# Kernel optimization log

Hardware: AMD Instinct MI355X
Metric: run time of the kernel (lower is better)

Reference implementation:

```python
import jax, jax.numpy as jnp
import numpy as np

HIDDEN = 1024
NUM_HEADS = 16
HEAD_DIM = HIDDEN // NUM_HEADS


def rotary_cos_sin(seq_len, head_dim, dtype=jnp.float32):
    inv_freq = 1.0 / (10000.0 ** (jnp.arange(0, head_dim, 2, dtype=dtype) / head_dim))
    t = jnp.arange(seq_len, dtype=dtype)
    freqs = jnp.einsum('i,j->ij', t, inv_freq)          # [S, hd/2]
    emb = jnp.concatenate([freqs, freqs], axis=-1)      # [S, hd]
    return jnp.cos(emb), jnp.sin(emb)


def apply_rotary(x, cos, sin):
    # x: [B, H, S, hd]; cos/sin: [S, hd]
    x1, x2 = jnp.split(x, 2, axis=-1)
    x_rot = jnp.concatenate([-x2, x1], axis=-1)
    return x * cos + x_rot * sin


def setup_inputs() -> dict:
    key = jax.random.key(0)
    ks = jax.random.split(key, 5)
    S, B = 2048, 2
    x = jax.random.normal(ks[0], (S, B, HIDDEN), dtype=jnp.float32)
    s = 1.0 / np.sqrt(HIDDEN)
    W_qkv = jax.random.uniform(ks[1], (HIDDEN, 3 * HIDDEN), jnp.float32, -s, s)
    b_qkv = jax.random.uniform(ks[2], (3 * HIDDEN,), jnp.float32, -s, s)
    W_out = jax.random.uniform(ks[3], (HIDDEN, HIDDEN), jnp.float32, -s, s)
    b_out = jax.random.uniform(ks[4], (HIDDEN,), jnp.float32, -s, s)
    return {"x": x, "W_qkv": W_qkv, "b_qkv": b_qkv, "W_out": W_out, "b_out": b_out}


def reference(x, W_qkv, b_qkv, W_out, b_out):
    S, B, D = x.shape
    scale = HEAD_DIM ** -0.5
    qkv = x @ W_qkv + b_qkv                               # [S, B, 3D]
    qkv = qkv.reshape(S, B, NUM_HEADS, 3 * HEAD_DIM)
    q, k, v = jnp.split(qkv, 3, axis=-1)                  # each [S, B, H, hd]
    q = q.transpose(1, 2, 0, 3)                           # [B, H, S, hd]
    k = k.transpose(1, 2, 0, 3)
    v = v.transpose(1, 2, 0, 3)
    cos, sin = rotary_cos_sin(S, HEAD_DIM, x.dtype)
    q = apply_rotary(q, cos, sin)
    k = apply_rotary(k, cos, sin)
    scores = jnp.einsum('bhqd,bhkd->bhqk', q, k) * scale  # [B, H, S, S]
    weights = jax.nn.softmax(scores, axis=-1)
    attn = jnp.einsum('bhqk,bhkd->bhqd', weights, v)      # [B, H, S, hd]
    attn = attn.transpose(2, 0, 1, 3).reshape(S, B, D)    # [S, B, D]
    return attn @ W_out + b_out
```

## Files before the change

kernel.cpp:

```cpp
#include <hip/hip_runtime.h>

typedef unsigned short u16;
typedef __attribute__((ext_vector_type(8))) short bf16x8;
typedef __attribute__((ext_vector_type(4))) float f32x4;
typedef __attribute__((ext_vector_type(16))) float f32x16;

#define S_LEN 2048
#define BATCH 2
#define HID 1024
#define NH 16
#define HD 64
#define MROWS 4096
#define QKV_N 3072
#define QSCALE 0.18033688011112042f

__device__ __forceinline__ u16 f2bf(float f) {
  unsigned u = __float_as_uint(f);
  u += 0x7fffu + ((u >> 16) & 1u);
  return (u16)(u >> 16);
}

__device__ __forceinline__ float bf2f(u16 u) {
  return __uint_as_float((unsigned)u << 16);
}

__device__ __forceinline__ float fexp2(float x) {
  float r; asm("v_exp_f32 %0, %1" : "=v"(r) : "v"(x)); return r;
}

__device__ __forceinline__ unsigned cvtpk(float lo, float hi) {
  unsigned r; asm("v_cvt_pk_bf16_f32 %0, %1, %2" : "=v"(r) : "v"(lo), "v"(hi)); return r;
}

__device__ __forceinline__ void gl2lds16(const u16* src, u16* lds) {
  __builtin_amdgcn_global_load_lds((__attribute__((address_space(1))) void*)(void*)src,
                                   (__attribute__((address_space(3))) void*)(void*)lds,
                                   16, 0, 0);
}

__device__ __forceinline__ void castT_body(const float* __restrict__ W, u16* __restrict__ Wt,
                                           int Ncols, int Krows, int bx, int by,
                                           float (*tile)[33]) {
  int c0 = bx * 32, r0 = by * 32;
  int tx = threadIdx.x & 31, ty = threadIdx.x >> 5;
  #pragma unroll
  for (int i = 0; i < 4; ++i)
    tile[ty + i * 8][tx] = W[(size_t)(r0 + ty + i * 8) * Ncols + c0 + tx];
  __syncthreads();
  #pragma unroll
  for (int i = 0; i < 4; ++i) {
    int a = ty + i * 8;
    Wt[(size_t)(c0 + a) * Krows + r0 + tx] = f2bf(tile[tx][a]);
  }
}

__global__ __launch_bounds__(256) void prep(
    const float* __restrict__ x, const float* __restrict__ W_qkv,
    const float* __restrict__ W_out, u16* __restrict__ xb,
    u16* __restrict__ Wqt, u16* __restrict__ Wot, float2* __restrict__ rope) {
  __shared__ float tile[32][33];
  const int bid = blockIdx.x;
  if (bid < 2048) {
    int i = bid * 256 + threadIdx.x;
    const float4* p = (const float4*)x;
    float4 a = p[2 * i], b = p[2 * i + 1];
    union { u16 us[8]; uint4 v; } o;
    o.us[0] = f2bf(a.x); o.us[1] = f2bf(a.y); o.us[2] = f2bf(a.z); o.us[3] = f2bf(a.w);
    o.us[4] = f2bf(b.x); o.us[5] = f2bf(b.y); o.us[6] = f2bf(b.z); o.us[7] = f2bf(b.w);
    *(uint4*)&xb[8 * i] = o.v;
  } else if (bid < 2048 + 3072) {
    int r = bid - 2048;
    castT_body(W_qkv, Wqt, QKV_N, HID, r % 96, r / 96, tile);
  } else if (bid < 2048 + 3072 + 1024) {
    int r = bid - (2048 + 3072);
    castT_body(W_out, Wot, HID, HID, r % 32, r / 32, tile);
  } else {
    int i = (bid - 6144) * 256 + threadIdx.x;
    int s = i >> 5, j = i & 31;
    float invf = fexp2(-(float)(2 * j) * (13.287712379549449f / 64.0f));
    float ang = (float)s * invf;
    rope[i] = make_float2(cosf(ang), sinf(ang));
  }
}

__global__ __launch_bounds__(256, 2) void gemm_qkv(
    const u16* __restrict__ A, const u16* __restrict__ Bt,
    const float* __restrict__ bias, const float2* __restrict__ rope,
    u16* __restrict__ Qb, u16* __restrict__ Kb, u16* __restrict__ VtOut) {
  __shared__ u16 As[128 * 32];
  __shared__ u16 Bs[128 * 32];
  __shared__ u16 vt[2][64][64];
  const int tid = threadIdx.x;
  const int lane = tid & 63, wid = tid >> 6;
  const int g = lane >> 4, l15 = lane & 15;
  const int bm0 = blockIdx.x * 128, bn0 = blockIdx.y * 128;
  const int wm = wid >> 1, wn = wid & 1;

  f32x4 acc[4][4] = {};
  for (int kt = 0; kt < 32; ++kt) {
    const int k0 = kt * 32;
    __syncthreads();
    #pragma unroll
    for (int it = 0; it < 2; ++it) {
      int s = it * 256 + tid;
      gl2lds16(A  + (size_t)(bm0 + (s >> 2)) * 1024 + k0 + (s & 3) * 8, &As[s * 8]);
      gl2lds16(Bt + (size_t)(bn0 + (s >> 2)) * 1024 + k0 + (s & 3) * 8, &Bs[s * 8]);
    }
    __syncthreads();
    bf16x8 af[4], bfr[4];
    #pragma unroll
    for (int m = 0; m < 4; ++m) af[m]  = *(const bf16x8*)&As[(wm * 64 + m * 16 + l15) * 32 + g * 8];
    #pragma unroll
    for (int n = 0; n < 4; ++n) bfr[n] = *(const bf16x8*)&Bs[(wn * 64 + n * 16 + l15) * 32 + g * 8];
    #pragma unroll
    for (int m = 0; m < 4; ++m)
      #pragma unroll
      for (int n = 0; n < 4; ++n)
        acc[m][n] = __builtin_amdgcn_mfma_f32_16x16x32_bf16(af[m], bfr[n], acc[m][n], 0, 0, 0);
  }

  const int cw0 = bn0 + wn * 64;
  const int gi = cw0 >> 6;
  const int h = gi / 3, tt = gi % 3;
  float bs[4];
  #pragma unroll
  for (int n = 0; n < 4; ++n) bs[n] = bias[cw0 + n * 16 + l15];
  const size_t hb = (size_t)h * (S_LEN * HD);

  if (tt == 2) {
    #pragma unroll
    for (int m = 0; m < 4; ++m)
      #pragma unroll
      for (int reg = 0; reg < 4; ++reg) {
        int rl = wm * 64 + m * 16 + g * 4 + reg;
        int srow = rl >> 1, b = reg & 1;
        #pragma unroll
        for (int n = 0; n < 4; ++n) {
          int d = n * 16 + l15;
          vt[b][d][srow ^ ((d & 7) << 3)] = f2bf(acc[m][n][reg] + bs[n]);
        }
      }
  } else {
    u16* dst = (tt == 0) ? Qb : Kb;
    const float scl = (tt == 0) ? QSCALE : 1.0f;
    #pragma unroll
    for (int m = 0; m < 4; ++m)
      #pragma unroll
      for (int reg = 0; reg < 4; ++reg) {
        int r = bm0 + wm * 64 + m * 16 + g * 4 + reg;
        int srow = r >> 1, b = r & 1;
        size_t o = (size_t)(b * NH) * (S_LEN * HD) + hb + (size_t)srow * HD;
        #pragma unroll
        for (int n = 0; n < 2; ++n) {
          int dlo = n * 16 + l15;
          float2 cs = rope[srow * 32 + dlo];
          float v1 = acc[m][n][reg] + bs[n];
          float v2 = acc[m][n + 2][reg] + bs[n + 2];
          dst[o + dlo]      = f2bf((v1 * cs.x - v2 * cs.y) * scl);
          dst[o + dlo + 32] = f2bf((v2 * cs.x + v1 * cs.y) * scl);
        }
      }
  }
  __syncthreads();
  if (tt == 2) {
    const int vtid = wm * 64 + lane;
    const int s0g = bm0 >> 1;
    #pragma unroll
    for (int it = 0; it < 8; ++it) {
      int task = vtid + it * 128;
      int b = task >> 9, d = (task >> 3) & 63, ch = task & 7;
      uint4 v = *(const uint4*)&vt[b][d][(ch ^ (d & 7)) * 8];
      *(uint4*)&VtOut[((size_t)(b * NH + h) * HD + d) * S_LEN + s0g + ch * 8] = v;
    }
  }
}

__global__ __launch_bounds__(512, 4) void attn_fwd(
    const u16* __restrict__ Qb, const u16* __restrict__ Kb,
    const u16* __restrict__ Vt, u16* __restrict__ part0,
    u16* __restrict__ part1, float2* __restrict__ stats) {
  __shared__ u16 Ks[2][64 * 64];
  __shared__ u16 Vs[2][64 * 64];
  const int tid = threadIdx.x;
  const int lane = tid & 63, wid = tid >> 6;
  const int l31 = lane & 31, h = lane >> 5;
  const int pp = blockIdx.x & 63;
  const int bh = pp >> 1, split = pp & 1;
  const int kt0 = split * 16;
  const int qw0 = (blockIdx.x >> 6) * 256 + wid * 32;
  const u16* Qp = Qb + ((size_t)bh * S_LEN + qw0) * HD;
  const u16* Kp = Kb + (size_t)bh * S_LEN * HD;
  const u16* Vp = Vt + (size_t)bh * HD * S_LEN;

  const int sr = tid >> 3, tc = tid & 7;
  const int ssw = tc ^ (sr & 7);
  const int act = ((sr >> 4) & 1) * 16 + ((sr >> 2) & 1) * 8
                + ((sr & 3) | (((sr >> 3) & 1) << 2)) + (sr >> 5) * 32;
  const u16* kg = Kp + (size_t)act * HD + ssw * 8;
  const u16* vg = Vp + (size_t)sr * S_LEN + ssw * 8;

  bf16x8 qf0 = *(const bf16x8*)&Qp[(size_t)l31 * HD +  0 + h * 8];
  bf16x8 qf1 = *(const bf16x8*)&Qp[(size_t)l31 * HD + 16 + h * 8];
  bf16x8 qf2 = *(const bf16x8*)&Qp[(size_t)l31 * HD + 32 + h * 8];
  bf16x8 qf3 = *(const bf16x8*)&Qp[(size_t)l31 * HD + 48 + h * 8];

  f32x16 po0 = {}, po1 = {};
  float mrun = -INFINITY, lrun = 0.f;

  gl2lds16(kg + (size_t)kt0 * 64 * HD, &Ks[0][tid * 8]);
  gl2lds16(vg + kt0 * 64, &Vs[0][tid * 8]);
  __syncthreads();

  for (int i = 0; i < 16; ++i) {
    const int bb = i & 1;
    if (i + 1 < 16) {
      gl2lds16(kg + (size_t)(kt0 + i + 1) * 64 * HD, &Ks[bb ^ 1][tid * 8]);
      gl2lds16(vg + (kt0 + i + 1) * 64, &Vs[bb ^ 1][tid * 8]);
    }
    const u16* KsB = Ks[bb];
    const u16* VsB = Vs[bb];

    f32x16 s0 = {}, s1 = {};
    __builtin_amdgcn_s_setprio(1);
    #pragma unroll
    for (int s = 0; s < 4; ++s) {
      const bf16x8 qf = (s == 0) ? qf0 : (s == 1) ? qf1 : (s == 2) ? qf2 : qf3;
      const int csw = ((2 * s + h) ^ (l31 & 7)) * 8;
      bf16x8 kf0 = *(const bf16x8*)&KsB[l31 * 64 + csw];
      s0 = __builtin_amdgcn_mfma_f32_32x32x16_bf16(kf0, qf, s0, 0, 0, 0);
      bf16x8 kf1 = *(const bf16x8*)&KsB[(32 + l31) * 64 + csw];
      s1 = __builtin_amdgcn_mfma_f32_32x32x16_bf16(kf1, qf, s1, 0, 0, 0);
    }
    __builtin_amdgcn_s_setprio(0);

    float tm = -INFINITY;
    #pragma unroll
    for (int r = 0; r < 16; ++r) tm = fmaxf(tm, fmaxf(s0[r], s1[r]));
    tm = fmaxf(tm, __shfl_xor(tm, 32));

    if (!__all(tm <= mrun + 8.f)) {
      float mnew = fmaxf(mrun, tm);
      float alpha = fexp2(mrun - mnew);
      mrun = mnew;
      lrun *= alpha;
      #pragma unroll
      for (int r = 0; r < 16; ++r) {
        float ar = __shfl(alpha, (r & 3) + 8 * (r >> 2) + 4 * h);
        po0[r] *= ar;
        po1[r] *= ar;
      }
    }

    float rs = 0.f;
    unsigned pwa[8], pwb[8];
    #pragma unroll
    for (int w = 0; w < 8; ++w) {
      float a = fexp2(s0[2 * w] - mrun), bq = fexp2(s0[2 * w + 1] - mrun);
      rs += a + bq;
      pwa[w] = cvtpk(a, bq);
    }
    #pragma unroll
    for (int w = 0; w < 8; ++w) {
      float a = fexp2(s1[2 * w] - mrun), bq = fexp2(s1[2 * w + 1] - mrun);
      rs += a + bq;
      pwb[w] = cvtpk(a, bq);
    }
    rs += __shfl_xor(rs, 32);
    lrun += rs;

    __builtin_amdgcn_s_setprio(1);
    #pragma unroll
    for (int s = 0; s < 4; ++s) {
      union { unsigned w[4]; bf16x8 v; } pf;
      if (s == 0)      { pf.w[0] = pwa[0]; pf.w[1] = pwa[1]; pf.w[2] = pwa[2]; pf.w[3] = pwa[3]; }
      else if (s == 1) { pf.w[0] = pwa[4]; pf.w[1] = pwa[5]; pf.w[2] = pwa[6]; pf.w[3] = pwa[7]; }
      else if (s == 2) { pf.w[0] = pwb[0]; pf.w[1] = pwb[1]; pf.w[2] = pwb[2]; pf.w[3] = pwb[3]; }
      else             { pf.w[0] = pwb[4]; pf.w[1] = pwb[5]; pf.w[2] = pwb[6]; pf.w[3] = pwb[7]; }
      const int csw = ((2 * s + h) ^ (l31 & 7)) * 8;
      bf16x8 vf0 = *(const bf16x8*)&VsB[l31 * 64 + csw];
      po0 = __builtin_amdgcn_mfma_f32_32x32x16_bf16(pf.v, vf0, po0, 0, 0, 0);
      bf16x8 vf1 = *(const bf16x8*)&VsB[(32 + l31) * 64 + csw];
      po1 = __builtin_amdgcn_mfma_f32_32x32x16_bf16(pf.v, vf1, po1, 0, 0, 0);
    }
    __builtin_amdgcn_s_setprio(0);
    __syncthreads();
  }

  u16* part = split ? part1 : part0;
  if (h == 0)
    stats[(size_t)split * (32 * 2048) + (size_t)bh * 2048 + qw0 + l31] =
        make_float2(mrun, lrun);
  #pragma unroll
  for (int r = 0; r < 16; ++r) {
    int q = qw0 + (r & 3) + 8 * (r >> 2) + 4 * h;
    size_t o = ((size_t)bh * 2048 + q) * 64 + l31;
    part[o]      = f2bf(po0[r]);
    part[o + 32] = f2bf(po1[r]);
  }
}

__global__ void attn_combine(const u16* __restrict__ part0, const u16* __restrict__ part1,
                             const float2* __restrict__ stats, u16* __restrict__ attn2d) {
  int t = blockIdx.x * 256 + threadIdx.x;
  int bh = t >> 14, r = t & 16383, q = r >> 3, dc = r & 7;
  int b = bh >> 4, h = bh & 15;
  float2 s0 = stats[bh * 2048 + q];
  float2 s1 = stats[32 * 2048 + bh * 2048 + q];
  float M = fmaxf(s0.x, s1.x);
  float w0 = fexp2(s0.x - M), w1 = fexp2(s1.x - M);
  float inv = 1.f / (w0 * s0.y + w1 * s1.y);
  w0 *= inv; w1 *= inv;
  size_t off = ((size_t)bh * 2048 + q) * 64 + dc * 8;
  union { uint4 v; u16 us[8]; } a, c, o;
  a.v = *(const uint4*)&part0[off];
  c.v = *(const uint4*)&part1[off];
  #pragma unroll
  for (int j = 0; j < 8; ++j)
    o.us[j] = f2bf(w0 * bf2f(a.us[j]) + w1 * bf2f(c.us[j]));
  *(uint4*)&attn2d[((size_t)q * BATCH + b) * HID + h * HD + dc * 8] = o.v;
}

__global__ __launch_bounds__(256, 4) void gemm_out(
    const u16* __restrict__ A, const u16* __restrict__ Bt,
    const float* __restrict__ bias, float* __restrict__ out) {
  __shared__ u16 As[64 * 32];
  __shared__ u16 Bs[64 * 32];
  const int tid = threadIdx.x;
  const int lane = tid & 63, wid = tid >> 6;
  const int g = lane >> 4, l15 = lane & 15;
  const int bm0 = blockIdx.x * 64, bn0 = blockIdx.y * 64;

  f32x4 acc[4] = {};
  for (int kt = 0; kt < 32; ++kt) {
    const int k0 = kt * 32;
    __syncthreads();
    gl2lds16(A  + (size_t)(bm0 + (tid >> 2)) * 1024 + k0 + (tid & 3) * 8, &As[tid * 8]);
    gl2lds16(Bt + (size_t)(bn0 + (tid >> 2)) * 1024 + k0 + (tid & 3) * 8, &Bs[tid * 8]);
    __syncthreads();
    bf16x8 af = *(const bf16x8*)&As[(wid * 16 + l15) * 32 + g * 8];
    bf16x8 bfr[4];
    #pragma unroll
    for (int n = 0; n < 4; ++n) bfr[n] = *(const bf16x8*)&Bs[(n * 16 + l15) * 32 + g * 8];
    #pragma unroll
    for (int n = 0; n < 4; ++n)
      acc[n] = __builtin_amdgcn_mfma_f32_16x16x32_bf16(af, bfr[n], acc[n], 0, 0, 0);
  }
  #pragma unroll
  for (int n = 0; n < 4; ++n) {
    int c = bn0 + n * 16 + l15;
    float bv = bias[c];
    #pragma unroll
    for (int reg = 0; reg < 4; ++reg) {
      int r = bm0 + wid * 16 + g * 4 + reg;
      out[(size_t)r * HID + c] = acc[n][reg] + bv;
    }
  }
}

extern "C" void kernel_launch(void* const* d_in, const int* in_sizes, int n_in,
                              void* d_out, int out_size, void* d_ws, size_t ws_size,
                              hipStream_t stream) {
  const float* x     = (const float*)d_in[0];
  const float* W_qkv = (const float*)d_in[1];
  const float* b_qkv = (const float*)d_in[2];
  const float* W_out = (const float*)d_in[3];
  const float* b_out = (const float*)d_in[4];
  float* out = (float*)d_out;

  char* ws = (char*)d_ws;
  size_t off = 0;
  auto carve = [&](size_t bytes) { void* p = ws + off; off += (bytes + 255) & ~(size_t)255; return p; };
  u16* xb      = (u16*)carve((size_t)MROWS * HID * 2);
  u16* Wqt     = (u16*)carve((size_t)QKV_N * HID * 2);
  u16* Wot     = (u16*)carve((size_t)HID * HID * 2);
  float2* rope = (float2*)carve((size_t)S_LEN * 32 * 8);
  u16* Qb      = (u16*)carve((size_t)BATCH * NH * S_LEN * HD * 2);
  u16* Kb      = (u16*)carve((size_t)BATCH * NH * S_LEN * HD * 2);
  u16* part1   = (u16*)carve((size_t)BATCH * NH * S_LEN * HD * 2);
  u16* Vt      = (u16*)carve((size_t)BATCH * NH * S_LEN * HD * 2);
  u16* attn2d  = (u16*)carve((size_t)MROWS * HID * 2);
  float2* stats= (float2*)carve((size_t)2 * 32 * 2048 * 8);

  prep<<<6400, 256, 0, stream>>>(x, W_qkv, W_out, xb, Wqt, Wot, rope);
  gemm_qkv<<<dim3(MROWS / 128, QKV_N / 128), 256, 0, stream>>>(xb, Wqt, b_qkv, rope, Qb, Kb, Vt);
  attn_fwd<<<512, 512, 0, stream>>>(Qb, Kb, Vt, xb, part1, stats);
  attn_combine<<<2048, 256, 0, stream>>>(xb, part1, stats, attn2d);
  gemm_out<<<dim3(MROWS / 64, HID / 64), 256, 0, stream>>>(attn2d, Wot, b_out, out);
}
```

Before: 120.7 us.

## Fuse split-KV combine into attention kernel via last-block atomic counter

Removes the separate attn_combine launch. Each attention block bumps an atomic counter per (query block, head), and whichever of the two split blocks finishes last merges both partial outputs and writes attn2d. Counters are zeroed in the prep kernel's rope blocks. This saves a kernel launch and its tail, but adds fences, an atomic, and a serialized combine tail on half of the blocks.

```diff
diff --git a/kernel.cpp b/kernel.cpp
--- a/kernel.cpp
+++ b/kernel.cpp
@@ -57,7 +57,8 @@
 __global__ __launch_bounds__(256) void prep(
     const float* __restrict__ x, const float* __restrict__ W_qkv,
     const float* __restrict__ W_out, u16* __restrict__ xb,
-    u16* __restrict__ Wqt, u16* __restrict__ Wot, float2* __restrict__ rope) {
+    u16* __restrict__ Wqt, u16* __restrict__ Wot, float2* __restrict__ rope,
+    int* __restrict__ flags) {
   __shared__ float tile[32][33];
   const int bid = blockIdx.x;
   if (bid < 2048) {
@@ -80,6 +81,7 @@
     float invf = fexp2(-(float)(2 * j) * (13.287712379549449f / 64.0f));
     float ang = (float)s * invf;
     rope[i] = make_float2(cosf(ang), sinf(ang));
+    if (threadIdx.x == 0) flags[bid - 6144] = 0;
   }
 }
 
@@ -178,16 +180,20 @@
 __global__ __launch_bounds__(512, 4) void attn_fwd(
     const u16* __restrict__ Qb, const u16* __restrict__ Kb,
     const u16* __restrict__ Vt, u16* __restrict__ part0,
-    u16* __restrict__ part1, float2* __restrict__ stats) {
+    u16* __restrict__ part1, float2* __restrict__ stats,
+    u16* __restrict__ attn2d, int* __restrict__ flags) {
   __shared__ u16 Ks[2][64 * 64];
   __shared__ u16 Vs[2][64 * 64];
+  __shared__ int lastflag;
   const int tid = threadIdx.x;
   const int lane = tid & 63, wid = tid >> 6;
   const int l31 = lane & 31, h = lane >> 5;
   const int pp = blockIdx.x & 63;
   const int bh = pp >> 1, split = pp & 1;
+  const int b = bh >> 4, head = bh & 15;
   const int kt0 = split * 16;
-  const int qw0 = (blockIdx.x >> 6) * 256 + wid * 32;
+  const int qb = blockIdx.x >> 6;
+  const int qw0 = qb * 256 + wid * 32;
   const u16* Qp = Qb + ((size_t)bh * S_LEN + qw0) * HD;
   const u16* Kp = Kb + (size_t)bh * S_LEN * HD;
   const u16* Vp = Vt + (size_t)bh * HD * S_LEN;
@@ -297,27 +303,36 @@
     part[o]      = f2bf(po0[r]);
     part[o + 32] = f2bf(po1[r]);
   }
-}
-
-__global__ void attn_combine(const u16* __restrict__ part0, const u16* __restrict__ part1,
-                             const float2* __restrict__ stats, u16* __restrict__ attn2d) {
-  int t = blockIdx.x * 256 + threadIdx.x;
-  int bh = t >> 14, r = t & 16383, q = r >> 3, dc = r & 7;
-  int b = bh >> 4, h = bh & 15;
-  float2 s0 = stats[bh * 2048 + q];
-  float2 s1 = stats[32 * 2048 + bh * 2048 + q];
-  float M = fmaxf(s0.x, s1.x);
-  float w0 = fexp2(s0.x - M), w1 = fexp2(s1.x - M);
-  float inv = 1.f / (w0 * s0.y + w1 * s1.y);
-  w0 *= inv; w1 *= inv;
-  size_t off = ((size_t)bh * 2048 + q) * 64 + dc * 8;
-  union { uint4 v; u16 us[8]; } a, c, o;
-  a.v = *(const uint4*)&part0[off];
-  c.v = *(const uint4*)&part1[off];
-  #pragma unroll
-  for (int j = 0; j < 8; ++j)
-    o.us[j] = f2bf(w0 * bf2f(a.us[j]) + w1 * bf2f(c.us[j]));
-  *(uint4*)&attn2d[((size_t)q * BATCH + b) * HID + h * HD + dc * 8] = o.v;
+
+  __threadfence();
+  __syncthreads();
+  if (tid == 0) lastflag = atomicAdd(&flags[qb * 32 + bh], 1);
+  __syncthreads();
+  if (lastflag == 1) {
+    __threadfence();
+    const size_t qbase = (size_t)bh * 2048 + qb * 256;
+    #pragma unroll
+    for (int it = 0; it < 4; ++it) {
+      int cid = it * 512 + tid;
+      int ql = cid >> 3, dc = cid & 7;
+      size_t qg = qbase + ql;
+      float2 st0 = stats[qg];
+      float2 st1 = stats[32 * 2048 + qg];
+      float M = fmaxf(st0.x, st1.x);
+      float w0 = fexp2(st0.x - M), w1 = fexp2(st1.x - M);
+      float inv = 1.f / (w0 * st0.y + w1 * st1.y);
+      w0 *= inv; w1 *= inv;
+      size_t o = qg * 64 + dc * 8;
+      union { uint4 v; u16 us[8]; } a, c2, ov;
+      a.v = *(const uint4*)&part0[o];
+      c2.v = *(const uint4*)&part1[o];
+      #pragma unroll
+      for (int j = 0; j < 8; ++j)
+        ov.us[j] = f2bf(w0 * bf2f(a.us[j]) + w1 * bf2f(c2.us[j]));
+      int q = qb * 256 + ql;
+      *(uint4*)&attn2d[((size_t)q * BATCH + b) * HID + head * HD + dc * 8] = ov.v;
+    }
+  }
 }
 
 __global__ __launch_bounds__(256, 4) void gemm_out(
@@ -380,10 +395,10 @@
   u16* Vt      = (u16*)carve((size_t)BATCH * NH * S_LEN * HD * 2);
   u16* attn2d  = (u16*)carve((size_t)MROWS * HID * 2);
   float2* stats= (float2*)carve((size_t)2 * 32 * 2048 * 8);
-
-  prep<<<6400, 256, 0, stream>>>(x, W_qkv, W_out, xb, Wqt, Wot, rope);
+  int* flags   = (int*)carve(256 * 4);
+
+  prep<<<6400, 256, 0, stream>>>(x, W_qkv, W_out, xb, Wqt, Wot, rope, flags);
   gemm_qkv<<<dim3(MROWS / 128, QKV_N / 128), 256, 0, stream>>>(xb, Wqt, b_qkv, rope, Qb, Kb, Vt);
-  attn_fwd<<<512, 512, 0, stream>>>(Qb, Kb, Vt, xb, part1, stats);
-  attn_combine<<<2048, 256, 0, stream>>>(xb, part1, stats, attn2d);
+  attn_fwd<<<512, 512, 0, stream>>>(Qb, Kb, Vt, xb, part1, stats, attn2d, flags);
   gemm_out<<<dim3(MROWS / 64, HID / 64), 256, 0, stream>>>(attn2d, Wot, b_out, out);
 }
```

Result: slower. 326.2 us (+170.2%).
